# Kernel optimization log

Measured on AMD Instinct MI355X. Metric: run time of the kernel, lower is better.

## Reference

```python
import jax, jax.numpy as jnp
import numpy as np

N_NODES = 10000
N_EDGES = 160000
D_IN = 50
ALPHA = 0.2  # LeakyReLU negative slope


def _xavier(key, shape):
    fan_in, fan_out = shape[0], int(np.prod(shape[1:]))
    limit = float(np.sqrt(6.0 / (fan_in + fan_out)))
    return jax.random.uniform(key, shape, jnp.float32, -limit, limit)


def setup_inputs() -> dict:
    key = jax.random.key(0)
    ks = jax.random.split(key, 8)
    x = jax.random.normal(ks[0], (N_NODES, D_IN), jnp.float32)
    edge_idx = jax.random.randint(ks[1], (2, N_EDGES), 0, N_NODES, jnp.int64)
    # layer 1: 50 -> 4 heads x 256, concat
    W1 = _xavier(ks[2], (D_IN, 4, 256))
    a1 = _xavier(ks[3], (4, 512))  # [H, 2F]: split into a_src, a_dst
    # layer 2: 1024 -> 4 heads x 256, concat
    W2 = _xavier(ks[4], (1024, 4, 256))
    a2 = _xavier(ks[5], (4, 512))
    # layer 3: 1024 -> 6 heads x 121, mean
    W3 = _xavier(ks[6], (1024, 6, 121))
    a3 = _xavier(ks[7], (6, 242))
    return {"x": x, "edge_idx": edge_idx, "W1": W1, "a1": a1,
            "W2": W2, "a2": a2, "W3": W3, "a3": a3}


def gat_layer(h, W, a, src, dst, aggregate):
    """Multi-head GAT layer over an edge list. h:[N,Din], W:[Din,H,F], a:[H,2F]."""
    N = h.shape[0]
    Wh = jnp.einsum('nd,dhf->nhf', h, W)                    # [N, H, F]
    F = Wh.shape[-1]
    att_src = jnp.einsum('nhf,hf->nh', Wh, a[:, :F])         # a^T [Wh_i || .]
    att_dst = jnp.einsum('nhf,hf->nh', Wh, a[:, F:])         # a^T [. || Wh_j]
    logits = jax.nn.leaky_relu(att_src[src] + att_dst[dst], ALPHA)  # [E, H]
    # numerically stable softmax over incoming edges of each destination node
    m = jax.ops.segment_max(logits, dst, num_segments=N)
    e = jnp.exp(logits - m[dst])
    denom = jax.ops.segment_sum(e, dst, num_segments=N)
    coef = e / (denom[dst] + 1e-16)                           # [E, H]
    out = jax.ops.segment_sum(coef[:, :, None] * Wh[src], dst, num_segments=N)
    if aggregate == 'concat':
        return out.reshape(N, -1)
    return out.mean(axis=1)


def reference(x, edge_idx, W1, a1, W2, a2, W3, a3):
    src, dst = edge_idx[0], edge_idx[1]
    h1 = jax.nn.elu(gat_layer(x, W1, a1, src, dst, 'concat'))   # [N, 1024]
    h2 = jax.nn.elu(gat_layer(h1, W2, a2, src, dst, 'concat'))  # [N, 1024]
    h3_in = h1 + h2                                              # residual skip
    return gat_layer(h3_in, W3, a3, src, dst, 'mean')            # [N, 121]
```

## Files before the change

### kernel.cpp

```cpp
#include <hip/hip_runtime.h>
#include <hip/hip_bf16.h>
#include <math.h>

#define NN 10000
#define NE 160000

typedef __attribute__((ext_vector_type(8))) _Float16 f16x8;
typedef __attribute__((ext_vector_type(4))) _Float16 f16x4;
typedef __attribute__((ext_vector_type(4))) float f32x4;

static __device__ __forceinline__ void gload_lds16(const _Float16* g, _Float16* l) {
  __builtin_amdgcn_global_load_lds((const __attribute__((address_space(1))) char*)g,
                                   (__attribute__((address_space(3))) char*)l, 16, 0, 0);
}

__global__ __launch_bounds__(1024) void scan_kernel(const int* __restrict__ counts,
                                                    int* __restrict__ row_ptr,
                                                    int* __restrict__ cursor, int N) {
  __shared__ int sums[1024];
  int t = threadIdx.x;
  const int CH = (N + 1023) >> 10;
  int base = t * CH;
  int s = 0;
  for (int i = 0; i < CH; ++i) { int idx = base + i; if (idx < N) s += counts[idx]; }
  sums[t] = s;
  __syncthreads();
  for (int off = 1; off < 1024; off <<= 1) {
    int v = 0;
    if (t >= off) v = sums[t - off];
    __syncthreads();
    if (t >= off) sums[t] += v;
    __syncthreads();
  }
  int run = (t == 0) ? 0 : sums[t - 1];
  for (int i = 0; i < CH; ++i) {
    int idx = base + i;
    if (idx < N) { row_ptr[idx] = run; cursor[idx] = run; run += counts[idx]; }
  }
  if (t == 0) row_ptr[N] = sums[1023];
}

__global__ void scatter_kernel(const int* __restrict__ src, const int* __restrict__ dst,
                               int* __restrict__ cursor, int* __restrict__ ssrc, int E) {
  int e = blockIdx.x * blockDim.x + threadIdx.x;
  if (e < E) {
    int pos = atomicAdd(&cursor[dst[e]], 1);
    ssrc[pos] = src[e];
  }
}

#define P0 (NN * 64)
#define P1 (1024 * 64)
#define P2 (1024 * 1024)
#define P3 (768 * 1024)
#define P4 NE
__global__ void prep_kernel(const float* __restrict__ x, const float* __restrict__ W1,
                            const float* __restrict__ W2, const float* __restrict__ W3,
                            const int* __restrict__ dst, int* __restrict__ counts,
                            _Float16* __restrict__ xh, _Float16* __restrict__ w1,
                            _Float16* __restrict__ w2, _Float16* __restrict__ w3) {
  int i = blockIdx.x * blockDim.x + threadIdx.x;
  if (i < P0) {
    int m = i >> 6, k = i & 63;
    xh[i] = (_Float16)(k < 50 ? x[m * 50 + k] : 0.f);
    return;
  }
  i -= P0;
  if (i < P1) {
    int n = i >> 6, k = i & 63;
    w1[i] = (_Float16)(k < 50 ? W1[k * 1024 + n] : 0.f);
    return;
  }
  i -= P1;
  if (i < P2) {
    int n = i >> 10, k = i & 1023;
    w2[i] = (_Float16)W2[k * 1024 + n];
    return;
  }
  i -= P2;
  if (i < P3) {
    int n = i >> 10, k = i & 1023;
    w3[i] = (_Float16)(n < 726 ? W3[k * 726 + n] : 0.f);
    return;
  }
  i -= P3;
  if (i < P4) atomicAdd(&counts[dst[i]], 1);
}

template<int PAD121>
__global__ __launch_bounds__(256) void gemm_f16(const _Float16* __restrict__ A,
                                                const _Float16* __restrict__ B,
                                                _Float16* __restrict__ C,
                                                int M, int KP, int NC) {
  int flat = blockIdx.x;
  int xcd = flat & 7;
  int slot = flat >> 3;
  int cblk = slot % NC;
  int rblk = (slot / NC) * 8 + xcd;
  const int m0 = rblk * 128;
  if (m0 >= M) return;
  const int n0 = cblk * 128;

  __shared__ _Float16 As[128 * 64];
  __shared__ _Float16 Bs[128 * 64];

  const int t = threadIdx.x;
  const int lane = t & 63;
  const int wid = t >> 6;
  const int wr = wid >> 1;
  const int wc = wid & 1;
  const int row_in = lane & 15;
  const int kgrp = lane >> 4;

  const int srow = wid * 32 + ((lane >> 3) & 7);
  const int sl7 = lane & 7;

  f32x4 acc[4][4];
#pragma unroll
  for (int i = 0; i < 4; ++i)
#pragma unroll
    for (int j = 0; j < 4; ++j) acc[i][j] = (f32x4){0.f, 0.f, 0.f, 0.f};

  for (int k0 = 0; k0 < KP; k0 += 64) {
    if (k0) __syncthreads();
#pragma unroll
    for (int j = 0; j < 4; ++j) {
      int row = srow + j * 8;
      int gs = (sl7 ^ (row & 7)) * 8;
      int gm = m0 + row;
      if (gm >= M) gm = M - 1;
      _Float16* ldsA = &As[(wid * 32 + j * 8) * 64];
      _Float16* ldsB = &Bs[(wid * 32 + j * 8) * 64];
      gload_lds16(&A[(size_t)gm * KP + k0 + gs], ldsA);
      gload_lds16(&B[(size_t)(n0 + row) * KP + k0 + gs], ldsB);
    }
    __syncthreads();

#pragma unroll
    for (int ks = 0; ks < 2; ++ks) {
      f16x8 a[4], b[4];
#pragma unroll
      for (int mi = 0; mi < 4; ++mi) {
        int arow = wr * 64 + mi * 16 + row_in;
        int ps = ((kgrp + ks * 4) ^ (arow & 7)) * 8;
        a[mi] = *(const f16x8*)&As[arow * 64 + ps];
      }
#pragma unroll
      for (int ni = 0; ni < 4; ++ni) {
        int brow = wc * 64 + ni * 16 + row_in;
        int ps = ((kgrp + ks * 4) ^ (brow & 7)) * 8;
        b[ni] = *(const f16x8*)&Bs[brow * 64 + ps];
      }
#pragma unroll
      for (int mi = 0; mi < 4; ++mi)
#pragma unroll
        for (int ni = 0; ni < 4; ++ni)
          acc[mi][ni] = __builtin_amdgcn_mfma_f32_16x16x32_f16(a[mi], b[ni], acc[mi][ni], 0, 0, 0);
    }
  }

#pragma unroll
  for (int mi = 0; mi < 4; ++mi) {
#pragma unroll
    for (int ni = 0; ni < 4; ++ni) {
      int gn = n0 + wc * 64 + ni * 16 + row_in;
#pragma unroll
      for (int j = 0; j < 4; ++j) {
        int gm = m0 + wr * 64 + mi * 16 + kgrp * 4 + j;
        if (gm >= M) continue;
        if (PAD121) {
          if (gn < 726) {
            int h = gn / 121;
            int pc = h * 128 + (gn - h * 121);
            C[(size_t)gm * 768 + pc] = (_Float16)acc[mi][ni][j];
          }
        } else {
          C[(size_t)gm * 1024 + gn] = (_Float16)acc[mi][ni][j];
        }
      }
    }
  }
}

template<int H, int F, int SW, int HS>
__global__ void att_kernel(const _Float16* __restrict__ Whb, const float* __restrict__ a,
                           float* __restrict__ att_s, float* __restrict__ att_d, int N) {
  int n = blockIdx.x;
  int h = threadIdx.x >> 6;
  int lane = threadIdx.x & 63;
  const _Float16* w = Whb + (size_t)n * SW + h * HS;
  const float* as = a + (size_t)h * 2 * F;
  const float* ad = as + F;
  float ss = 0.f, sd = 0.f;
  for (int f = lane; f < F; f += 64) {
    float v = (float)w[f];
    ss += v * as[f];
    sd += v * ad[f];
  }
#pragma unroll
  for (int off = 32; off > 0; off >>= 1) {
    ss += __shfl_down(ss, off);
    sd += __shfl_down(sd, off);
  }
  if (lane == 0) {
    att_s[n * H + h] = ss;
    att_d[n * H + h] = sd;
  }
}

template<int H>
__global__ __launch_bounds__(64) void edge_softmax_csr(const int* __restrict__ row_ptr,
                                                       const int* __restrict__ ssrc,
                                                       const float* __restrict__ att_s,
                                                       const float* __restrict__ att_d,
                                                       float* __restrict__ cbuf,
                                                       float* __restrict__ dinv, int N) {
  int n = blockIdx.x;
  int lane = threadIdx.x;
  int beg = row_ptr[n], end = row_ptr[n + 1];
  float ad[H];
#pragma unroll
  for (int h = 0; h < H; ++h) ad[h] = att_d[n * H + h];

  float m[H];
#pragma unroll
  for (int h = 0; h < H; ++h) m[h] = -INFINITY;
  for (int k = beg + lane; k < end; k += 64) {
    int s = ssrc[k];
#pragma unroll
    for (int h = 0; h < H; ++h) {
      float x = att_s[s * H + h] + ad[h];
      float l = x >= 0.f ? x : 0.2f * x;
      m[h] = fmaxf(m[h], l);
    }
  }
#pragma unroll
  for (int h = 0; h < H; ++h)
#pragma unroll
    for (int off = 32; off > 0; off >>= 1) m[h] = fmaxf(m[h], __shfl_xor(m[h], off));

  float sum[H];
#pragma unroll
  for (int h = 0; h < H; ++h) sum[h] = 0.f;
  for (int k = beg + lane; k < end; k += 64) {
    int s = ssrc[k];
#pragma unroll
    for (int h = 0; h < H; ++h) {
      float x = att_s[s * H + h] + ad[h];
      float l = x >= 0.f ? x : 0.2f * x;
      float ev = __expf(l - m[h]);
      cbuf[(size_t)k * H + h] = ev;
      sum[h] += ev;
    }
  }
#pragma unroll
  for (int h = 0; h < H; ++h) {
#pragma unroll
    for (int off = 32; off > 0; off >>= 1) sum[h] += __shfl_xor(sum[h], off);
  }
  if (lane < H) dinv[n * H + lane] = 1.f / (sum[lane] + 1e-16f);
}

template<int MODE>
__global__ __launch_bounds__(256) void aggregate_cat_chunk(const int* __restrict__ row_ptr,
                                                           const int* __restrict__ ssrc,
                                                           const float* __restrict__ cbuf,
                                                           const float* __restrict__ dinv,
                                                           const _Float16* __restrict__ Whb,
                                                           const _Float16* __restrict__ h1,
                                                           _Float16* __restrict__ outv, int N) {
  int b = blockIdx.x;
  int chunk = b & 7;
  int group = b >> 3;
  int n = group * 16 + (threadIdx.x >> 4);
  if (n >= N) return;
  int tt = threadIdx.x & 15;
  int idx = chunk * 128 + tt * 8;
  int h = chunk >> 1;
  float inv = dinv[n * 4 + h];

  float acc[8] = {};
  int beg = row_ptr[n], end = row_ptr[n + 1];
  int k = beg;
  for (; k + 1 < end; k += 2) {
    int s0 = ssrc[k], s1 = ssrc[k + 1];
    float c0 = cbuf[(size_t)k * 4 + h];
    float c1 = cbuf[(size_t)(k + 1) * 4 + h];
    f16x8 w0 = *(const f16x8*)&Whb[(size_t)s0 * 1024 + idx];
    f16x8 w1 = *(const f16x8*)&Whb[(size_t)s1 * 1024 + idx];
#pragma unroll
    for (int j = 0; j < 8; ++j) {
      acc[j] += c0 * (float)w0[j];
      acc[j] += c1 * (float)w1[j];
    }
  }
  if (k < end) {
    int s0 = ssrc[k];
    float c0 = cbuf[(size_t)k * 4 + h];
    f16x8 w0 = *(const f16x8*)&Whb[(size_t)s0 * 1024 + idx];
#pragma unroll
    for (int j = 0; j < 8; ++j) acc[j] += c0 * (float)w0[j];
  }

  size_t o = (size_t)n * 1024 + idx;
  f16x8 r1;
  if (MODE == 1) r1 = *(const f16x8*)&h1[o];
  f16x8 vo;
#pragma unroll
  for (int j = 0; j < 8; ++j) {
    float v = acc[j] * inv;
    v = v > 0.f ? v : expm1f(v);
    if (MODE == 1) v += (float)r1[j];
    vo[j] = (_Float16)v;
  }
  *(f16x8*)&outv[o] = vo;
}

__global__ __launch_bounds__(256) void aggregate_mean_chunk(const int* __restrict__ row_ptr,
                                                            const int* __restrict__ ssrc,
                                                            const float* __restrict__ cbuf,
                                                            const float* __restrict__ dinv,
                                                            const _Float16* __restrict__ Whb,
                                                            float* __restrict__ part, int N) {
  int b = blockIdx.x;
  int h = b & 7;
  if (h >= 6) return;
  int n = (b >> 3) * 16 + (threadIdx.x >> 4);
  if (n >= N) return;
  int tt = threadIdx.x & 15;
  int base = h * 128 + tt * 8;
  float inv = dinv[n * 6 + h];

  float acc[8] = {};
  int beg = row_ptr[n], end = row_ptr[n + 1];
  int k = beg;
  for (; k + 1 < end; k += 2) {
    int s0 = ssrc[k], s1 = ssrc[k + 1];
    float c0 = cbuf[(size_t)k * 6 + h];
    float c1 = cbuf[(size_t)(k + 1) * 6 + h];
    f16x8 w0 = *(const f16x8*)&Whb[(size_t)s0 * 768 + base];
    f16x8 w1 = *(const f16x8*)&Whb[(size_t)s1 * 768 + base];
#pragma unroll
    for (int j = 0; j < 8; ++j) {
      acc[j] += c0 * (float)w0[j];
      acc[j] += c1 * (float)w1[j];
    }
  }
  if (k < end) {
    int s0 = ssrc[k];
    float c0 = cbuf[(size_t)k * 6 + h];
    f16x8 w0 = *(const f16x8*)&Whb[(size_t)s0 * 768 + base];
#pragma unroll
    for (int j = 0; j < 8; ++j) acc[j] += c0 * (float)w0[j];
  }

  float* p = &part[(size_t)n * 768 + base];
  *(f32x4*)&p[0] = (f32x4){acc[0] * inv, acc[1] * inv, acc[2] * inv, acc[3] * inv};
  *(f32x4*)&p[4] = (f32x4){acc[4] * inv, acc[5] * inv, acc[6] * inv, acc[7] * inv};
}

__global__ __launch_bounds__(128) void reduce_mean(const float* __restrict__ part,
                                                   float* __restrict__ out, int N) {
  int n = blockIdx.x;
  int f = threadIdx.x;
  if (f >= 121) return;
  const float* p = &part[(size_t)n * 768];
  float s = 0.f;
#pragma unroll
  for (int h = 0; h < 6; ++h) s += p[h * 128 + f];
  out[(size_t)n * 121 + f] = s * (1.0f / 6.0f);
}

extern "C" void kernel_launch(void* const* d_in, const int* in_sizes, int n_in,
                              void* d_out, int out_size, void* d_ws, size_t ws_size,
                              hipStream_t stream) {
  const float* x  = (const float*)d_in[0];
  const int* eidx = (const int*)d_in[1];
  const float* W1 = (const float*)d_in[2];
  const float* a1 = (const float*)d_in[3];
  const float* W2 = (const float*)d_in[4];
  const float* a2 = (const float*)d_in[5];
  const float* W3 = (const float*)d_in[6];
  const float* a3 = (const float*)d_in[7];
  float* out = (float*)d_out;

  const int N = NN, E = NE;
  const int* src = eidx;
  const int* dst = eidx + E;

  char* ws = (char*)d_ws;
  size_t off = 0;
  auto alloc = [&](size_t bytes) -> void* {
    void* p = ws + off;
    off += (bytes + 255) & ~(size_t)255;
    return p;
  };
  _Float16* Whf  = (_Float16*)alloc((size_t)N * 1024 * 2);
  _Float16* h1   = (_Float16*)alloc((size_t)N * 1024 * 2);
  _Float16* hsum = (_Float16*)alloc((size_t)N * 1024 * 2);
  _Float16* xh   = (_Float16*)alloc((size_t)N * 64 * 2);
  _Float16* w1   = (_Float16*)alloc((size_t)1024 * 64 * 2);
  _Float16* w2   = (_Float16*)alloc((size_t)1024 * 1024 * 2);
  _Float16* w3   = (_Float16*)alloc((size_t)768 * 1024 * 2);
  float* cbuf  = (float*)alloc((size_t)E * 6 * 4);
  float* part  = (float*)alloc((size_t)N * 768 * 4);
  float* atts  = (float*)alloc((size_t)N * 6 * 4);
  float* attd  = (float*)alloc((size_t)N * 6 * 4);
  float* dinv  = (float*)alloc((size_t)N * 6 * 4);
  int* counts  = (int*)alloc((size_t)N * 4);
  int* row_ptr = (int*)alloc((size_t)(N + 1) * 4);
  int* cursor  = (int*)alloc((size_t)N * 4);
  int* ssrc    = (int*)alloc((size_t)E * 4);

  hipMemsetAsync(counts, 0, (size_t)N * 4, stream);
  const int PTOT = P0 + P1 + P2 + P3 + P4;
  prep_kernel<<<(PTOT + 255) / 256, 256, 0, stream>>>(x, W1, W2, W3, dst, counts, xh, w1, w2, w3);
  scan_kernel<<<1, 1024, 0, stream>>>(counts, row_ptr, cursor, N);
  scatter_kernel<<<(E + 255) / 256, 256, 0, stream>>>(src, dst, cursor, ssrc, E);

  const int RPG = 10;
  const int AGG_GRID = 8 * ((N + 15) / 16);

  gemm_f16<0><<<8 * RPG * 8, 256, 0, stream>>>(xh, w1, Whf, N, 64, 8);
  att_kernel<4, 256, 1024, 256><<<N, 256, 0, stream>>>(Whf, a1, atts, attd, N);
  edge_softmax_csr<4><<<N, 64, 0, stream>>>(row_ptr, ssrc, atts, attd, cbuf, dinv, N);
  aggregate_cat_chunk<0><<<AGG_GRID, 256, 0, stream>>>(row_ptr, ssrc, cbuf, dinv, Whf, nullptr, h1, N);

  gemm_f16<0><<<8 * RPG * 8, 256, 0, stream>>>(h1, w2, Whf, N, 1024, 8);
  att_kernel<4, 256, 1024, 256><<<N, 256, 0, stream>>>(Whf, a2, atts, attd, N);
  edge_softmax_csr<4><<<N, 64, 0, stream>>>(row_ptr, ssrc, atts, attd, cbuf, dinv, N);
  aggregate_cat_chunk<1><<<AGG_GRID, 256, 0, stream>>>(row_ptr, ssrc, cbuf, dinv, Whf, h1, hsum, N);

  gemm_f16<1><<<8 * RPG * 6, 256, 0, stream>>>(hsum, w3, Whf, N, 1024, 6);
  att_kernel<6, 121, 768, 128><<<N, 384, 0, stream>>>(Whf, a3, atts, attd, N);
  edge_softmax_csr<6><<<N, 64, 0, stream>>>(row_ptr, ssrc, atts, attd, cbuf, dinv, N);
  aggregate_mean_chunk<<<AGG_GRID, 256, 0, stream>>>(row_ptr, ssrc, cbuf, dinv, Whf, part, N);
  reduce_mean<<<N, 128, 0, stream>>>(part, out, N);
}
```

Baseline: 289.3 us.

## Tile weight transposes through LDS and pack 16 nodes per softmax block

The weight prep kernel now transposes W1/W2/W3 through a 64x65 shared-memory tile, so both the fp32 reads and the fp16 writes are coalesced instead of strided global reads. The edge softmax kernel switches from one 64-lane block per node to 16 lanes per node with 16 nodes per 256-thread block. With an average degree of 16 this leaves fewer lanes idle, and it uses vectorized float4 loads and stores for the 4-head case. Fewer lanes per node can serialize work on high-degree nodes, and the float4 accesses assume 16-byte alignment of the attention and coefficient buffers.

Measured after the change: 276.7 us. 1.05x faster.

```diff
diff --git a/kernel.cpp b/kernel.cpp
--- a/kernel.cpp
+++ b/kernel.cpp
@@ -49,42 +49,65 @@
   }
 }
 
-#define P0 (NN * 64)
-#define P1 (1024 * 64)
-#define P2 (1024 * 1024)
-#define P3 (768 * 1024)
-#define P4 NE
-__global__ void prep_kernel(const float* __restrict__ x, const float* __restrict__ W1,
-                            const float* __restrict__ W2, const float* __restrict__ W3,
-                            const int* __restrict__ dst, int* __restrict__ counts,
-                            _Float16* __restrict__ xh, _Float16* __restrict__ w1,
-                            _Float16* __restrict__ w2, _Float16* __restrict__ w3) {
-  int i = blockIdx.x * blockDim.x + threadIdx.x;
-  if (i < P0) {
+#define TB_W2 256
+#define TB_W3 192
+#define TB_W1 16
+#define TB_T (TB_W2 + TB_W3 + TB_W1)
+#define TB_X ((NN * 64) / 256)
+#define TB_E ((NE + 255) / 256)
+__global__ __launch_bounds__(256) void prep2(const float* __restrict__ x,
+                                             const float* __restrict__ W1,
+                                             const float* __restrict__ W2,
+                                             const float* __restrict__ W3,
+                                             const int* __restrict__ dst,
+                                             int* __restrict__ counts,
+                                             _Float16* __restrict__ xh,
+                                             _Float16* __restrict__ w1,
+                                             _Float16* __restrict__ w2,
+                                             _Float16* __restrict__ w3) {
+  int b = blockIdx.x;
+  int t = threadIdx.x;
+  if (b < TB_T) {
+    const float* S;
+    _Float16* D;
+    int K, Nsrc, KP, k0, n0;
+    if (b < TB_W2) {
+      S = W2; D = w2; K = 1024; Nsrc = 1024; KP = 1024;
+      k0 = (b & 15) * 64; n0 = (b >> 4) * 64;
+    } else if (b < TB_W2 + TB_W3) {
+      int bb = b - TB_W2;
+      S = W3; D = w3; K = 1024; Nsrc = 726; KP = 1024;
+      k0 = (bb & 15) * 64; n0 = (bb >> 4) * 64;
+    } else {
+      int bb = b - TB_W2 - TB_W3;
+      S = W1; D = w1; K = 50; Nsrc = 1024; KP = 64;
+      k0 = 0; n0 = bb * 64;
+    }
+    __shared__ float tile[64][65];
+#pragma unroll
+    for (int i = 0; i < 16; ++i) {
+      int idx = i * 256 + t;
+      int r = idx >> 6, c = idx & 63;
+      int gk = k0 + r, gn = n0 + c;
+      tile[r][c] = (gk < K && gn < Nsrc) ? S[(size_t)gk * Nsrc + gn] : 0.f;
+    }
+    __syncthreads();
+#pragma unroll
+    for (int i = 0; i < 16; ++i) {
+      int idx = i * 256 + t;
+      int r = idx >> 6, c = idx & 63;
+      D[(size_t)(n0 + r) * KP + k0 + c] = (_Float16)tile[c][r];
+    }
+    return;
+  }
+  int i = (b - TB_T) * 256 + t;
+  if (i < NN * 64) {
     int m = i >> 6, k = i & 63;
     xh[i] = (_Float16)(k < 50 ? x[m * 50 + k] : 0.f);
     return;
   }
-  i -= P0;
-  if (i < P1) {
-    int n = i >> 6, k = i & 63;
-    w1[i] = (_Float16)(k < 50 ? W1[k * 1024 + n] : 0.f);
-    return;
-  }
-  i -= P1;
-  if (i < P2) {
-    int n = i >> 10, k = i & 1023;
-    w2[i] = (_Float16)W2[k * 1024 + n];
-    return;
-  }
-  i -= P2;
-  if (i < P3) {
-    int n = i >> 10, k = i & 1023;
-    w3[i] = (_Float16)(n < 726 ? W3[k * 726 + n] : 0.f);
-    return;
-  }
-  i -= P3;
-  if (i < P4) atomicAdd(&counts[dst[i]], 1);
+  i -= NN * 64;
+  if (i < NE) atomicAdd(&counts[dst[i]], 1);
 }
 
 template<int PAD121>
@@ -209,54 +232,83 @@
 }
 
 template<int H>
-__global__ __launch_bounds__(64) void edge_softmax_csr(const int* __restrict__ row_ptr,
-                                                       const int* __restrict__ ssrc,
-                                                       const float* __restrict__ att_s,
-                                                       const float* __restrict__ att_d,
-                                                       float* __restrict__ cbuf,
-                                                       float* __restrict__ dinv, int N) {
-  int n = blockIdx.x;
-  int lane = threadIdx.x;
+__global__ __launch_bounds__(256) void edge_softmax_csr(const int* __restrict__ row_ptr,
+                                                        const int* __restrict__ ssrc,
+                                                        const float* __restrict__ att_s,
+                                                        const float* __restrict__ att_d,
+                                                        float* __restrict__ cbuf,
+                                                        float* __restrict__ dinv, int N) {
+  int n = blockIdx.x * 16 + (threadIdx.x >> 4);
+  if (n >= N) return;
+  int lane = threadIdx.x & 15;
   int beg = row_ptr[n], end = row_ptr[n + 1];
+
   float ad[H];
-#pragma unroll
-  for (int h = 0; h < H; ++h) ad[h] = att_d[n * H + h];
+  if (H == 4) {
+    f32x4 v = *(const f32x4*)&att_d[n * 4];
+    ad[0] = v.x; ad[1] = v.y; ad[2] = v.z; ad[3] = v.w;
+  } else {
+#pragma unroll
+    for (int h = 0; h < H; ++h) ad[h] = att_d[n * H + h];
+  }
 
   float m[H];
 #pragma unroll
   for (int h = 0; h < H; ++h) m[h] = -INFINITY;
-  for (int k = beg + lane; k < end; k += 64) {
+  for (int k = beg + lane; k < end; k += 16) {
     int s = ssrc[k];
+    float as[H];
+    if (H == 4) {
+      f32x4 v = *(const f32x4*)&att_s[s * 4];
+      as[0] = v.x; as[1] = v.y; as[2] = v.z; as[3] = v.w;
+    } else {
+#pragma unroll
+      for (int h = 0; h < H; ++h) as[h] = att_s[s * H + h];
+    }
 #pragma unroll
     for (int h = 0; h < H; ++h) {
-      float x = att_s[s * H + h] + ad[h];
-      float l = x >= 0.f ? x : 0.2f * x;
+      float xv = as[h] + ad[h];
+      float l = xv >= 0.f ? xv : 0.2f * xv;
       m[h] = fmaxf(m[h], l);
     }
   }
 #pragma unroll
   for (int h = 0; h < H; ++h)
 #pragma unroll
-    for (int off = 32; off > 0; off >>= 1) m[h] = fmaxf(m[h], __shfl_xor(m[h], off));
+    for (int off = 8; off > 0; off >>= 1) m[h] = fmaxf(m[h], __shfl_xor(m[h], off));
 
   float sum[H];
 #pragma unroll
   for (int h = 0; h < H; ++h) sum[h] = 0.f;
-  for (int k = beg + lane; k < end; k += 64) {
+  for (int k = beg + lane; k < end; k += 16) {
     int s = ssrc[k];
+    float as[H];
+    if (H == 4) {
+      f32x4 v = *(const f32x4*)&att_s[s * 4];
+      as[0] = v.x; as[1] = v.y; as[2] = v.z; as[3] = v.w;
+    } else {
+#pragma unroll
+      for (int h = 0; h < H; ++h) as[h] = att_s[s * H + h];
+    }
+    float ev[H];
 #pragma unroll
     for (int h = 0; h < H; ++h) {
-      float x = att_s[s * H + h] + ad[h];
-      float l = x >= 0.f ? x : 0.2f * x;
-      float ev = __expf(l - m[h]);
-      cbuf[(size_t)k * H + h] = ev;
-      sum[h] += ev;
+      float xv = as[h] + ad[h];
+      float l = xv >= 0.f ? xv : 0.2f * xv;
+      ev[h] = __expf(l - m[h]);
+      sum[h] += ev[h];
+    }
+    if (H == 4) {
+      *(f32x4*)&cbuf[(size_t)k * 4] = (f32x4){ev[0], ev[1], ev[2], ev[3]};
+    } else {
+#pragma unroll
+      for (int h = 0; h < H; ++h) cbuf[(size_t)k * H + h] = ev[h];
     }
   }
 #pragma unroll
   for (int h = 0; h < H; ++h) {
 #pragma unroll
-    for (int off = 32; off > 0; off >>= 1) sum[h] += __shfl_xor(sum[h], off);
+    for (int off = 8; off > 0; off >>= 1) sum[h] += __shfl_xor(sum[h], off);
   }
   if (lane < H) dinv[n * H + lane] = 1.f / (sum[lane] + 1e-16f);
 }
@@ -413,27 +465,27 @@
   int* ssrc    = (int*)alloc((size_t)E * 4);
 
   hipMemsetAsync(counts, 0, (size_t)N * 4, stream);
-  const int PTOT = P0 + P1 + P2 + P3 + P4;
-  prep_kernel<<<(PTOT + 255) / 256, 256, 0, stream>>>(x, W1, W2, W3, dst, counts, xh, w1, w2, w3);
+  prep2<<<TB_T + TB_X + TB_E, 256, 0, stream>>>(x, W1, W2, W3, dst, counts, xh, w1, w2, w3);
   scan_kernel<<<1, 1024, 0, stream>>>(counts, row_ptr, cursor, N);
   scatter_kernel<<<(E + 255) / 256, 256, 0, stream>>>(src, dst, cursor, ssrc, E);
 
   const int RPG = 10;
   const int AGG_GRID = 8 * ((N + 15) / 16);
+  const int SM_GRID = (N + 15) / 16;
 
   gemm_f16<0><<<8 * RPG * 8, 256, 0, stream>>>(xh, w1, Whf, N, 64, 8);
   att_kernel<4, 256, 1024, 256><<<N, 256, 0, stream>>>(Whf, a1, atts, attd, N);
-  edge_softmax_csr<4><<<N, 64, 0, stream>>>(row_ptr, ssrc, atts, attd, cbuf, dinv, N);
+  edge_softmax_csr<4><<<SM_GRID, 256, 0, stream>>>(row_ptr, ssrc, atts, attd, cbuf, dinv, N);
   aggregate_cat_chunk<0><<<AGG_GRID, 256, 0, stream>>>(row_ptr, ssrc, cbuf, dinv, Whf, nullptr, h1, N);
 
   gemm_f16<0><<<8 * RPG * 8, 256, 0, stream>>>(h1, w2, Whf, N, 1024, 8);
   att_kernel<4, 256, 1024, 256><<<N, 256, 0, stream>>>(Whf, a2, atts, attd, N);
-  edge_softmax_csr<4><<<N, 64, 0, stream>>>(row_ptr, ssrc, atts, attd, cbuf, dinv, N);
+  edge_softmax_csr<4><<<SM_GRID, 256, 0, stream>>>(row_ptr, ssrc, atts, attd, cbuf, dinv, N);
   aggregate_cat_chunk<1><<<AGG_GRID, 256, 0, stream>>>(row_ptr, ssrc, cbuf, dinv, Whf, h1, hsum, N);
 
   gemm_f16<1><<<8 * RPG * 6, 256, 0, stream>>>(hsum, w3, Whf, N, 1024, 6);
   att_kernel<6, 121, 768, 128><<<N, 384, 0, stream>>>(Whf, a3, atts, attd, N);
-  edge_softmax_csr<6><<<N, 64, 0, stream>>>(row_ptr, ssrc, atts, attd, cbuf, dinv, N);
+  edge_softmax_csr<6><<<SM_GRID, 256, 0, stream>>>(row_ptr, ssrc, atts, attd, cbuf, dinv, N);
   aggregate_mean_chunk<<<AGG_GRID, 256, 0, stream>>>(row_ptr, ssrc, cbuf, dinv, Whf, part, N);
   reduce_mean<<<N, 128, 0, stream>>>(part, out, N);
 }
```
